# Kernel optimization log

Hardware: AMD Instinct MI355X
Metric: run time of the kernel (lower is better)

## Reference

```python
import jax, jax.numpy as jnp
import numpy as np

N = 50000   # nodes
E = 800000  # random edges (self-loops appended inside reference, as PyG GATConv does)
H = 4       # attention heads
LEAKY_SLOPE = 0.2
BN_EPS = 1e-5


def setup_inputs() -> dict:
    key = jax.random.key(0)
    ks = jax.random.split(key, 24)
    inp = {
        "x": jax.random.normal(ks[0], (N, 128), jnp.float32),
        "edge_index": jax.random.randint(ks[1], (2, E), 0, N, dtype=jnp.int64),
    }
    # layer dims: (in, out_per_head); concat -> out width = H*out
    dims = [(128, 64), (256, 64), (256, 32)]
    i = 2
    for l, (fin, c) in enumerate(dims, start=1):
        sc = 1.0 / np.sqrt(fin)
        inp[f"W{l}"] = jax.random.normal(ks[i], (fin, H * c), jnp.float32) * sc; i += 1
        inp[f"a_src{l}"] = jax.random.normal(ks[i], (H, c), jnp.float32) * 0.1; i += 1
        inp[f"a_dst{l}"] = jax.random.normal(ks[i], (H, c), jnp.float32) * 0.1; i += 1
        inp[f"b{l}"] = jnp.zeros((H * c,), jnp.float32)
    # batch norm params for the two non-final layers (width = 64*4 = 256)
    for l in (1, 2):
        inp[f"gamma{l}"] = jnp.ones((256,), jnp.float32)
        inp[f"beta{l}"] = jnp.zeros((256,), jnp.float32)
    return inp


def _gat_layer(x, src, dst, W, a_src, a_dst, b, heads):
    n = x.shape[0]
    h = (x @ W).reshape(n, heads, -1)                      # [N,H,C]
    al_s = jnp.sum(h * a_src, axis=-1)                     # [N,H]
    al_d = jnp.sum(h * a_dst, axis=-1)                     # [N,H]
    e = jax.nn.leaky_relu(al_s[src] + al_d[dst], LEAKY_SLOPE)  # [Etot,H]
    # numerically-stable edge softmax over incoming edges per destination
    m = jax.ops.segment_max(e, dst, num_segments=n)
    e = jnp.exp(e - m[dst])
    s = jax.ops.segment_sum(e, dst, num_segments=n)
    alpha = e / (s[dst] + 1e-16)                           # [Etot,H]
    msg = alpha[:, :, None] * h[src]                       # [Etot,H,C]
    out = jax.ops.segment_sum(msg, dst, num_segments=n)    # [N,H,C]
    out = out.reshape(n, -1) + b
    return jax.nn.relu(out)  # GAT_NET applies relu after conv


def _batch_norm(x, gamma, beta):
    mean = jnp.mean(x, axis=0)
    var = jnp.var(x, axis=0)  # biased, matches torch BN training normalization
    return (x - mean) * jax.lax.rsqrt(var + BN_EPS) * gamma + beta


def reference(x, edge_index, W1, a_src1, a_dst1, b1, gamma1, beta1,
              W2, a_src2, a_dst2, b2, gamma2, beta2,
              W3, a_src3, a_dst3, b3):
    n = x.shape[0]
    loop = jnp.arange(n, dtype=edge_index.dtype)
    src = jnp.concatenate([edge_index[0], loop])  # add self-loops (PyG default)
    dst = jnp.concatenate([edge_index[1], loop])

    h = _gat_layer(x, src, dst, W1, a_src1, a_dst1, b1, H)
    # outer F.relu is a no-op after GAT_NET's internal relu, kept implicitly
    h = _batch_norm(h, gamma1, beta1)

    h = _gat_layer(h, src, dst, W2, a_src2, a_dst2, b2, H)
    h = _batch_norm(h, gamma2, beta2)

    return _gat_layer(h, src, dst, W3, a_src3, a_dst3, b3, H)
```

## Files before the change

### kernel.cpp

```cpp
#include <hip/hip_runtime.h>
#include <hip/hip_bf16.h>

constexpr int NN   = 50000;
constexpr int EE   = 800000;
constexpr int ETOT = EE + NN;
constexpr int NP   = 50048;
constexpr int NBLK = (NN + 255) / 256;
constexpr float SLOPE  = 0.2f;
constexpr float EPS_BN = 1e-5f;

typedef __attribute__((ext_vector_type(8))) short bf16x8;
typedef __attribute__((ext_vector_type(4))) float f32x4;

__device__ inline float bf2f(unsigned short u) {
    union { unsigned int i; float f; } c; c.i = ((unsigned int)u) << 16; return c.f;
}

__device__ inline void gload16(const __hip_bfloat16* g, __hip_bfloat16* l) {
    __builtin_amdgcn_global_load_lds(
        (const __attribute__((address_space(1))) unsigned int*)g,
        (__attribute__((address_space(3))) unsigned int*)l, 16, 0, 0);
}


__global__ __launch_bounds__(256) void count_kernel(const int* __restrict__ ei,
                                                    int* __restrict__ cnt) {
    int j = blockIdx.x * 256 + threadIdx.x;
    if (j >= ETOT) return;
    int dst = (j < EE) ? ei[EE + j] : (j - EE);
    atomicAdd(&cnt[dst], 1);
}

__global__ __launch_bounds__(256) void scanA_kernel(const int* __restrict__ cnt,
                                                    int* __restrict__ off,
                                                    int* __restrict__ bsum) {
    int b = blockIdx.x, t = threadIdx.x;
    int i = b * 256 + t;
    int v = (i < NN) ? cnt[i] : 0;
    int lane = t & 63, w = t >> 6;
    int x = v;
    #pragma unroll
    for (int o = 1; o < 64; o <<= 1) { int y = __shfl_up(x, o); if (lane >= o) x += y; }
    __shared__ int ws[4];
    if (lane == 63) ws[w] = x;
    __syncthreads();
    int wo = 0;
    for (int k = 0; k < w; ++k) wo += ws[k];
    int incl = x + wo;
    if (i < NN) off[i] = incl - v;
    if (t == 255) bsum[b] = incl;
}

__global__ __launch_bounds__(256) void scanB_kernel(const int* __restrict__ bsum,
                                                    int* __restrict__ bexc,
                                                    int* __restrict__ off) {
    int t = threadIdx.x;
    int v = (t < NBLK) ? bsum[t] : 0;
    int lane = t & 63, w = t >> 6;
    int x = v;
    #pragma unroll
    for (int o = 1; o < 64; o <<= 1) { int y = __shfl_up(x, o); if (lane >= o) x += y; }
    __shared__ int ws[4];
    if (lane == 63) ws[w] = x;
    __syncthreads();
    int wo = 0;
    for (int k = 0; k < w; ++k) wo += ws[k];
    int incl = x + wo;
    if (t < NBLK) bexc[t] = incl - v;
    if (t == 255) off[NN] = incl;
}

__global__ __launch_bounds__(256) void scanC_kernel(const int* __restrict__ bexc,
                                                    int* __restrict__ off,
                                                    int* __restrict__ cur) {
    int i = blockIdx.x * 256 + threadIdx.x;
    if (i >= NN) return;
    int v = off[i] + bexc[blockIdx.x];
    off[i] = v;
    cur[i] = v;
}

__global__ __launch_bounds__(256) void fill_kernel(const int* __restrict__ ei,
                                                   int* __restrict__ cursor,
                                                   int* __restrict__ ssrc) {
    int j = blockIdx.x * 256 + threadIdx.x;
    if (j >= ETOT) return;
    int src, dst;
    if (j < EE) { src = ei[j]; dst = ei[EE + j]; }
    else        { src = dst = j - EE; }
    int pos = atomicAdd(&cursor[dst], 1);
    ssrc[pos] = src;
}

template <int F, bool BN>
__global__ __launch_bounds__(256) void cast_kernel(const float* __restrict__ X,
                                                   const float* __restrict__ scale,
                                                   const float* __restrict__ shift,
                                                   __hip_bfloat16* __restrict__ Xbf) {
    long idx = (long)blockIdx.x * 256 + threadIdx.x;
    long e0 = idx * 8;
    if (e0 >= (long)NP * F) return;
    int row = (int)(e0 / F);
    int col = (int)(e0 % F);
    __hip_bfloat16 o[8];
    if (row < NN) {
        float4 v0 = *reinterpret_cast<const float4*>(X + (size_t)row * F + col);
        float4 v1 = *reinterpret_cast<const float4*>(X + (size_t)row * F + col + 4);
        if (BN) {
            float4 s0 = *reinterpret_cast<const float4*>(scale + col);
            float4 s1 = *reinterpret_cast<const float4*>(scale + col + 4);
            float4 t0 = *reinterpret_cast<const float4*>(shift + col);
            float4 t1 = *reinterpret_cast<const float4*>(shift + col + 4);
            v0.x = v0.x * s0.x + t0.x; v0.y = v0.y * s0.y + t0.y;
            v0.z = v0.z * s0.z + t0.z; v0.w = v0.w * s0.w + t0.w;
            v1.x = v1.x * s1.x + t1.x; v1.y = v1.y * s1.y + t1.y;
            v1.z = v1.z * s1.z + t1.z; v1.w = v1.w * s1.w + t1.w;
        }
        o[0] = __float2bfloat16(v0.x); o[1] = __float2bfloat16(v0.y);
        o[2] = __float2bfloat16(v0.z); o[3] = __float2bfloat16(v0.w);
        o[4] = __float2bfloat16(v1.x); o[5] = __float2bfloat16(v1.y);
        o[6] = __float2bfloat16(v1.z); o[7] = __float2bfloat16(v1.w);
    } else {
        for (int j = 0; j < 8; ++j) o[j] = __float2bfloat16(0.f);
    }
    *reinterpret_cast<bf16x8*>(Xbf + e0) = *reinterpret_cast<bf16x8*>(o);
}

__global__ __launch_bounds__(256) void castw_all_kernel(const float* __restrict__ W1,
                                                        const float* __restrict__ W2,
                                                        const float* __restrict__ W3,
                                                        __hip_bfloat16* __restrict__ WT1,
                                                        __hip_bfloat16* __restrict__ WT2,
                                                        __hip_bfloat16* __restrict__ WT3) {
    int i = blockIdx.x * 256 + threadIdx.x;
    if (i < 32768) {
        int c = i / 128, k = i % 128;
        WT1[i] = __float2bfloat16(W1[(size_t)k * 256 + c]);
    } else if (i < 98304) {
        int j = i - 32768;
        int c = j / 256, k = j % 256;
        WT2[j] = __float2bfloat16(W2[(size_t)k * 256 + c]);
    } else if (i < 131072) {
        int j = i - 98304;
        int c = j / 256, k = j % 256;
        WT3[j] = __float2bfloat16(W3[(size_t)k * 128 + c]);
    }
}

template <int FIN, int WOUT>
__global__ __launch_bounds__(256) void mgemm_kernel(const __hip_bfloat16* __restrict__ A,
                                                    const __hip_bfloat16* __restrict__ BT,
                                                    __hip_bfloat16* __restrict__ Hbf) {
    __shared__ __hip_bfloat16 As[128 * 32];
    __shared__ __hip_bfloat16 Bs[128 * 32];
    int t = threadIdx.x;
    int lane = t & 63, w = t >> 6;
    int row0 = blockIdx.x * 128;
    int col0 = blockIdx.y * 128;
    int wr = w >> 1, wc = w & 1;

    f32x4 acc[4][4];
    #pragma unroll
    for (int m = 0; m < 4; ++m)
        #pragma unroll
        for (int n = 0; n < 4; ++n) acc[m][n] = (f32x4){0.f, 0.f, 0.f, 0.f};

    int srow = w * 32 + (lane >> 2);
    int sbc  = (lane & 3) * 8;
    const __hip_bfloat16* gA0 = A  + (size_t)(row0 + srow)      * FIN + sbc;
    const __hip_bfloat16* gA1 = A  + (size_t)(row0 + srow + 16) * FIN + sbc;
    const __hip_bfloat16* gB0 = BT + (size_t)(col0 + srow)      * FIN + sbc;
    const __hip_bfloat16* gB1 = BT + (size_t)(col0 + srow + 16) * FIN + sbc;
    __hip_bfloat16* lA0 = As + w * 1024;
    __hip_bfloat16* lA1 = As + w * 1024 + 512;
    __hip_bfloat16* lB0 = Bs + w * 1024;
    __hip_bfloat16* lB1 = Bs + w * 1024 + 512;

    int rA = (wr * 64 + (lane & 15)) * 32 + (lane >> 4) * 8;
    int rB = (wc * 64 + (lane & 15)) * 32 + (lane >> 4) * 8;

    for (int k0 = 0; k0 < FIN; k0 += 32) {
        gload16(gA0 + k0, lA0);
        gload16(gA1 + k0, lA1);
        gload16(gB0 + k0, lB0);
        gload16(gB1 + k0, lB1);
        __syncthreads();
        bf16x8 af[4], bfr[4];
        #pragma unroll
        for (int m = 0; m < 4; ++m) af[m]  = *reinterpret_cast<const bf16x8*>(As + rA + m * 16 * 32);
        #pragma unroll
        for (int n = 0; n < 4; ++n) bfr[n] = *reinterpret_cast<const bf16x8*>(Bs + rB + n * 16 * 32);
        #pragma unroll
        for (int m = 0; m < 4; ++m)
            #pragma unroll
            for (int n = 0; n < 4; ++n)
                acc[m][n] = __builtin_amdgcn_mfma_f32_16x16x32_bf16(af[m], bfr[n], acc[m][n], 0, 0, 0);
        __syncthreads();
    }

    #pragma unroll
    for (int m = 0; m < 4; ++m) {
        #pragma unroll
        for (int n = 0; n < 4; ++n) {
            int r = row0 + wr * 64 + m * 16 + (lane >> 4) * 4;
            int c = col0 + wc * 64 + n * 16 + (lane & 15);
            #pragma unroll
            for (int j = 0; j < 4; ++j)
                Hbf[(size_t)(r + j) * WOUT + c] = __float2bfloat16(acc[m][n][j]);
        }
    }
}

template <int HC>
__global__ __launch_bounds__(256) void alsd_kernel(const __hip_bfloat16* __restrict__ Hm,
                                                   const float* __restrict__ a_src,
                                                   const float* __restrict__ a_dst,
                                                   float* __restrict__ als,
                                                   float* __restrict__ ald) {
    constexpr int VW = HC / 64;
    int wid  = threadIdx.x >> 6;
    int lane = threadIdx.x & 63;
    int node = blockIdx.x * 4 + wid;

    float ssum = 0.f, dsum = 0.f;
    if constexpr (VW == 4) {
        ushort4 h4 = *reinterpret_cast<const ushort4*>(Hm + (size_t)node * HC + lane * 4);
        float4 as = *reinterpret_cast<const float4*>(a_src + lane * 4);
        float4 ad = *reinterpret_cast<const float4*>(a_dst + lane * 4);
        float hx = bf2f(h4.x), hy = bf2f(h4.y), hz = bf2f(h4.z), hw = bf2f(h4.w);
        ssum = hx*as.x + hy*as.y + hz*as.z + hw*as.w;
        dsum = hx*ad.x + hy*ad.y + hz*ad.z + hw*ad.w;
    } else {
        ushort2 h2 = *reinterpret_cast<const ushort2*>(Hm + (size_t)node * HC + lane * 2);
        float2 as = *reinterpret_cast<const float2*>(a_src + lane * 2);
        float2 ad = *reinterpret_cast<const float2*>(a_dst + lane * 2);
        float hx = bf2f(h2.x), hy = bf2f(h2.y);
        ssum = hx*as.x + hy*as.y;
        dsum = hx*ad.x + hy*ad.y;
    }
    #pragma unroll
    for (int o = 1; o < 16; o <<= 1) {
        ssum += __shfl_xor(ssum, o);
        dsum += __shfl_xor(dsum, o);
    }
    if ((lane & 15) == 0) {
        int hd = lane >> 4;
        als[node * 4 + hd] = ssum;
        ald[node * 4 + hd] = dsum;
    }
}

template <int HC>
__global__ __launch_bounds__(256) void attn_kernel(const __hip_bfloat16* __restrict__ Hm,
                                                   const int* __restrict__ off,
                                                   const int* __restrict__ ssrc,
                                                   const float* __restrict__ als,
                                                   const float* __restrict__ ald,
                                                   const float* __restrict__ bias,
                                                   float* __restrict__ Out) {
    constexpr int CPL = HC / 16;
    int wid  = threadIdx.x >> 6;
    int lane = threadIdx.x & 63;
    int d    = blockIdx.x * 4 + wid;
    int g    = lane >> 4;
    int q    = lane & 15;
    int head = q >> 2;

    int e0 = off[d], e1 = off[d + 1];
    float aldh = ald[(size_t)d * 4 + head];

    float acc[CPL];
    #pragma unroll
    for (int c = 0; c < CPL; ++c) acc[c] = 0.f;
    float den = 0.f;

    for (int j = e0 + g; j < e1; j += 4) {
        int src = ssrc[j];
        float e = als[(size_t)src * 4 + head] + aldh;
        e = (e > 0.f) ? e : SLOPE * e;
        float wgt = __expf(e);
        den += wgt;
        const __hip_bfloat16* hp = Hm + (size_t)src * HC + q * CPL;
        if constexpr (CPL == 16) {
            bf16x8 v0 = *reinterpret_cast<const bf16x8*>(hp);
            bf16x8 v1 = *reinterpret_cast<const bf16x8*>(hp + 8);
            #pragma unroll
            for (int c = 0; c < 8; ++c) acc[c]     += wgt * bf2f((unsigned short)v0[c]);
            #pragma unroll
            for (int c = 0; c < 8; ++c) acc[8 + c] += wgt * bf2f((unsigned short)v1[c]);
        } else {
            bf16x8 v0 = *reinterpret_cast<const bf16x8*>(hp);
            #pragma unroll
            for (int c = 0; c < 8; ++c) acc[c] += wgt * bf2f((unsigned short)v0[c]);
        }
    }

    #pragma unroll
    for (int c = 0; c < CPL; ++c) {
        acc[c] += __shfl_xor(acc[c], 16);
        acc[c] += __shfl_xor(acc[c], 32);
    }
    den += __shfl_xor(den, 16);
    den += __shfl_xor(den, 32);
    float inv = 1.f / (den + 1e-16f);

    if (g == 0) {
        #pragma unroll
        for (int c4 = 0; c4 < CPL / 4; ++c4) {
            float4 b4 = *reinterpret_cast<const float4*>(bias + q * CPL + c4 * 4);
            float4 o;
            o.x = fmaxf(acc[c4 * 4 + 0] * inv + b4.x, 0.f);
            o.y = fmaxf(acc[c4 * 4 + 1] * inv + b4.y, 0.f);
            o.z = fmaxf(acc[c4 * 4 + 2] * inv + b4.z, 0.f);
            o.w = fmaxf(acc[c4 * 4 + 3] * inv + b4.w, 0.f);
            *reinterpret_cast<float4*>(Out + (size_t)d * HC + q * CPL + c4 * 4) = o;
        }
    }
}

__global__ __launch_bounds__(256) void bnstats_kernel(const float* __restrict__ X,
                                                      float* __restrict__ sums) {
    int c  = threadIdx.x;
    int r0 = blockIdx.x * 200;
    float s = 0.f, q = 0.f;
    for (int r = r0; r < r0 + 200; ++r) {
        float v = X[(size_t)r * 256 + c];
        s += v; q += v * v;
    }
    atomicAdd(&sums[c], s);
    atomicAdd(&sums[256 + c], q);
}

__global__ __launch_bounds__(256) void bnfinal_kernel(const float* __restrict__ sums,
                                                      const float* __restrict__ gamma,
                                                      const float* __restrict__ beta,
                                                      float* __restrict__ scale,
                                                      float* __restrict__ shift) {
    int c = threadIdx.x;
    float mean = sums[c] / (float)NN;
    float var  = sums[256 + c] / (float)NN - mean * mean;
    float inv  = rsqrtf(var + EPS_BN);
    float sc   = gamma[c] * inv;
    scale[c] = sc;
    shift[c] = beta[c] - mean * sc;
}


extern "C" void kernel_launch(void* const* d_in, const int* in_sizes, int n_in,
                              void* d_out, int out_size, void* d_ws, size_t ws_size,
                              hipStream_t stream) {
    const float* x      = (const float*)d_in[0];
    const int*   ei     = (const int*)d_in[1];
    const float* W1     = (const float*)d_in[2];
    const float* a_s1   = (const float*)d_in[3];
    const float* a_d1   = (const float*)d_in[4];
    const float* b1     = (const float*)d_in[5];
    const float* W2     = (const float*)d_in[6];
    const float* a_s2   = (const float*)d_in[7];
    const float* a_d2   = (const float*)d_in[8];
    const float* b2     = (const float*)d_in[9];
    const float* W3     = (const float*)d_in[10];
    const float* a_s3   = (const float*)d_in[11];
    const float* a_d3   = (const float*)d_in[12];
    const float* b3     = (const float*)d_in[13];
    const float* gamma1 = (const float*)d_in[14];
    const float* beta1  = (const float*)d_in[15];
    const float* gamma2 = (const float*)d_in[16];
    const float* beta2  = (const float*)d_in[17];

    char* ws = (char*)d_ws;
    size_t o = 0;
    auto alloc = [&](size_t bytes) -> void* {
        void* p = ws + o;
        o = (o + bytes + 255) & ~size_t(255);
        return p;
    };
    float*           bufB = (float*)alloc((size_t)NN * 256 * 4);
    __hip_bfloat16*  Xbf  = (__hip_bfloat16*)alloc((size_t)NP * 256 * 2);
    __hip_bfloat16*  Hbf  = (__hip_bfloat16*)alloc((size_t)NP * 256 * 2);
    __hip_bfloat16*  WT1  = (__hip_bfloat16*)alloc((size_t)256 * 128 * 2);
    __hip_bfloat16*  WT2  = (__hip_bfloat16*)alloc((size_t)256 * 256 * 2);
    __hip_bfloat16*  WT3  = (__hip_bfloat16*)alloc((size_t)128 * 256 * 2);
    float* als   = (float*)alloc((size_t)NN * 4 * 4);
    float* ald   = (float*)alloc((size_t)NN * 4 * 4);
    float* sums  = (float*)alloc(512 * 4);
    float* scale = (float*)alloc(256 * 4);
    float* shift = (float*)alloc(256 * 4);
    int*   off   = (int*)alloc((size_t)(NN + 1) * 4);
    int*   cur   = (int*)alloc((size_t)NN * 4);
    int*   cnt   = (int*)alloc((size_t)NN * 4);
    int*   bsum  = (int*)alloc((size_t)NBLK * 4);
    int*   bexc  = (int*)alloc((size_t)NBLK * 4);
    int*   ssrc  = (int*)alloc((size_t)ETOT * 4);
    (void)ws_size; (void)in_sizes; (void)n_in; (void)out_size;

    const int EB = (ETOT + 255) / 256;

    hipMemsetAsync(cnt, 0, (size_t)NN * 4, stream);
    count_kernel<<<EB, 256, 0, stream>>>(ei, cnt);
    scanA_kernel<<<NBLK, 256, 0, stream>>>(cnt, off, bsum);
    scanB_kernel<<<1, 256, 0, stream>>>(bsum, bexc, off);
    scanC_kernel<<<NBLK, 256, 0, stream>>>(bexc, off, cur);
    fill_kernel<<<EB, 256, 0, stream>>>(ei, cur, ssrc);

    castw_all_kernel<<<512, 256, 0, stream>>>(W1, W2, W3, WT1, WT2, WT3);

    cast_kernel<128, false><<<(int)(((long)NP * 128 / 8 + 255) / 256), 256, 0, stream>>>(x, nullptr, nullptr, Xbf);
    mgemm_kernel<128, 256><<<dim3(NP / 128, 2), 256, 0, stream>>>(Xbf, WT1, Hbf);
    alsd_kernel<256><<<NN / 4, 256, 0, stream>>>(Hbf, a_s1, a_d1, als, ald);
    attn_kernel<256><<<NN / 4, 256, 0, stream>>>(Hbf, off, ssrc, als, ald, b1, bufB);

    hipMemsetAsync(sums, 0, 512 * 4, stream);
    bnstats_kernel<<<250, 256, 0, stream>>>(bufB, sums);
    bnfinal_kernel<<<1, 256, 0, stream>>>(sums, gamma1, beta1, scale, shift);

    cast_kernel<256, true><<<(int)(((long)NP * 256 / 8 + 255) / 256), 256, 0, stream>>>(bufB, scale, shift, Xbf);
    mgemm_kernel<256, 256><<<dim3(NP / 128, 2), 256, 0, stream>>>(Xbf, WT2, Hbf);
    alsd_kernel<256><<<NN / 4, 256, 0, stream>>>(Hbf, a_s2, a_d2, als, ald);
    attn_kernel<256><<<NN / 4, 256, 0, stream>>>(Hbf, off, ssrc, als, ald, b2, bufB);

    hipMemsetAsync(sums, 0, 512 * 4, stream);
    bnstats_kernel<<<250, 256, 0, stream>>>(bufB, sums);
    bnfinal_kernel<<<1, 256, 0, stream>>>(sums, gamma2, beta2, scale, shift);

    cast_kernel<256, true><<<(int)(((long)NP * 256 / 8 + 255) / 256), 256, 0, stream>>>(bufB, scale, shift, Xbf);
    mgemm_kernel<256, 128><<<dim3(NP / 128, 1), 256, 0, stream>>>(Xbf, WT3, Hbf);
    alsd_kernel<128><<<NN / 4, 256, 0, stream>>>(Hbf, a_s3, a_d3, als, ald);
    attn_kernel<128><<<NN / 4, 256, 0, stream>>>(Hbf, off, ssrc, als, ald, b3, (float*)d_out);
}
```

Before: 413.6 us.

## Fold batch-norm into next-layer weights and emit bf16 attention outputs

Batch-norm scale and shift are folded into the next layer's weight matrix and a per-column bias added in the GEMM epilogue. This removes the separate normalize-and-cast passes over the activation buffer. The intermediate attention outputs are now written directly as bf16, halving their write traffic, and bnstats reads bf16. The attention edge loop is also unrolled by two with independent accumulators to expose more memory-level parallelism. Risks: BN statistics are computed from bf16-rounded values, and the folded weights are rounded to bf16 after scaling.

```diff
diff --git a/kernel.cpp b/kernel.cpp
--- a/kernel.cpp
+++ b/kernel.cpp
@@ -92,30 +92,15 @@
     ssrc[pos] = src;
 }
 
-template <int F, bool BN>
-__global__ __launch_bounds__(256) void cast_kernel(const float* __restrict__ X,
-                                                   const float* __restrict__ scale,
-                                                   const float* __restrict__ shift,
-                                                   __hip_bfloat16* __restrict__ Xbf) {
-    long idx = (long)blockIdx.x * 256 + threadIdx.x;
-    long e0 = idx * 8;
-    if (e0 >= (long)NP * F) return;
-    int row = (int)(e0 / F);
-    int col = (int)(e0 % F);
+__global__ __launch_bounds__(256) void castx_kernel(const float* __restrict__ X,
+                                                    __hip_bfloat16* __restrict__ Xbf) {
+    long e0 = ((long)blockIdx.x * 256 + threadIdx.x) * 8;
+    if (e0 >= (long)NP * 128) return;
+    int row = (int)(e0 / 128);
     __hip_bfloat16 o[8];
     if (row < NN) {
-        float4 v0 = *reinterpret_cast<const float4*>(X + (size_t)row * F + col);
-        float4 v1 = *reinterpret_cast<const float4*>(X + (size_t)row * F + col + 4);
-        if (BN) {
-            float4 s0 = *reinterpret_cast<const float4*>(scale + col);
-            float4 s1 = *reinterpret_cast<const float4*>(scale + col + 4);
-            float4 t0 = *reinterpret_cast<const float4*>(shift + col);
-            float4 t1 = *reinterpret_cast<const float4*>(shift + col + 4);
-            v0.x = v0.x * s0.x + t0.x; v0.y = v0.y * s0.y + t0.y;
-            v0.z = v0.z * s0.z + t0.z; v0.w = v0.w * s0.w + t0.w;
-            v1.x = v1.x * s1.x + t1.x; v1.y = v1.y * s1.y + t1.y;
-            v1.z = v1.z * s1.z + t1.z; v1.w = v1.w * s1.w + t1.w;
-        }
+        float4 v0 = *reinterpret_cast<const float4*>(X + e0);
+        float4 v1 = *reinterpret_cast<const float4*>(X + e0 + 4);
         o[0] = __float2bfloat16(v0.x); o[1] = __float2bfloat16(v0.y);
         o[2] = __float2bfloat16(v0.z); o[3] = __float2bfloat16(v0.w);
         o[4] = __float2bfloat16(v1.x); o[5] = __float2bfloat16(v1.y);
@@ -126,30 +111,41 @@
     *reinterpret_cast<bf16x8*>(Xbf + e0) = *reinterpret_cast<bf16x8*>(o);
 }
 
-__global__ __launch_bounds__(256) void castw_all_kernel(const float* __restrict__ W1,
-                                                        const float* __restrict__ W2,
-                                                        const float* __restrict__ W3,
-                                                        __hip_bfloat16* __restrict__ WT1,
-                                                        __hip_bfloat16* __restrict__ WT2,
-                                                        __hip_bfloat16* __restrict__ WT3) {
+__global__ __launch_bounds__(256) void castw1_kernel(const float* __restrict__ W,
+                                                     __hip_bfloat16* __restrict__ WT) {
     int i = blockIdx.x * 256 + threadIdx.x;
-    if (i < 32768) {
-        int c = i / 128, k = i % 128;
-        WT1[i] = __float2bfloat16(W1[(size_t)k * 256 + c]);
-    } else if (i < 98304) {
-        int j = i - 32768;
-        int c = j / 256, k = j % 256;
-        WT2[j] = __float2bfloat16(W2[(size_t)k * 256 + c]);
-    } else if (i < 131072) {
-        int j = i - 98304;
-        int c = j / 256, k = j % 256;
-        WT3[j] = __float2bfloat16(W3[(size_t)k * 128 + c]);
-    }
+    if (i >= 32768) return;
+    int c = i / 128, k = i % 128;
+    WT[i] = __float2bfloat16(W[(size_t)k * 256 + c]);
 }
 
 template <int FIN, int WOUT>
+__global__ __launch_bounds__(FIN) void foldw_kernel(const float* __restrict__ W,
+                                                    const float* __restrict__ scale,
+                                                    const float* __restrict__ shift,
+                                                    __hip_bfloat16* __restrict__ WTp,
+                                                    float* __restrict__ bb) {
+    int c = blockIdx.x, k = threadIdx.x;
+    float w = W[(size_t)k * WOUT + c];
+    WTp[(size_t)c * FIN + k] = __float2bfloat16(scale[k] * w);
+    float p = shift[k] * w;
+    #pragma unroll
+    for (int o = 1; o < 64; o <<= 1) p += __shfl_xor(p, o);
+    __shared__ float ps[FIN / 64];
+    if ((k & 63) == 0) ps[k >> 6] = p;
+    __syncthreads();
+    if (k == 0) {
+        float s = 0.f;
+        #pragma unroll
+        for (int q = 0; q < FIN / 64; ++q) s += ps[q];
+        bb[c] = s;
+    }
+}
+
+template <int FIN, int WOUT, bool FOLD>
 __global__ __launch_bounds__(256) void mgemm_kernel(const __hip_bfloat16* __restrict__ A,
                                                     const __hip_bfloat16* __restrict__ BT,
+                                                    const float* __restrict__ bb,
                                                     __hip_bfloat16* __restrict__ Hbf) {
     __shared__ __hip_bfloat16 As[128 * 32];
     __shared__ __hip_bfloat16 Bs[128 * 32];
@@ -199,14 +195,15 @@
     }
 
     #pragma unroll
-    for (int m = 0; m < 4; ++m) {
-        #pragma unroll
-        for (int n = 0; n < 4; ++n) {
+    for (int n = 0; n < 4; ++n) {
+        int c = col0 + wc * 64 + n * 16 + (lane & 15);
+        float badd = FOLD ? bb[c] : 0.f;
+        #pragma unroll
+        for (int m = 0; m < 4; ++m) {
             int r = row0 + wr * 64 + m * 16 + (lane >> 4) * 4;
-            int c = col0 + wc * 64 + n * 16 + (lane & 15);
             #pragma unroll
             for (int j = 0; j < 4; ++j)
-                Hbf[(size_t)(r + j) * WOUT + c] = __float2bfloat16(acc[m][n][j]);
+                Hbf[(size_t)(r + j) * WOUT + c] = __float2bfloat16(acc[m][n][j] + badd);
         }
     }
 }
@@ -250,14 +247,14 @@
     }
 }
 
-template <int HC>
+template <int HC, bool OUTBF>
 __global__ __launch_bounds__(256) void attn_kernel(const __hip_bfloat16* __restrict__ Hm,
                                                    const int* __restrict__ off,
                                                    const int* __restrict__ ssrc,
                                                    const float* __restrict__ als,
                                                    const float* __restrict__ ald,
                                                    const float* __restrict__ bias,
-                                                   float* __restrict__ Out) {
+                                                   void* __restrict__ Outv) {
     constexpr int CPL = HC / 16;
     int wid  = threadIdx.x >> 6;
     int lane = threadIdx.x & 63;
@@ -269,31 +266,71 @@
     int e0 = off[d], e1 = off[d + 1];
     float aldh = ald[(size_t)d * 4 + head];
 
+    float acc0[CPL], acc1[CPL];
+    #pragma unroll
+    for (int c = 0; c < CPL; ++c) { acc0[c] = 0.f; acc1[c] = 0.f; }
+    float den0 = 0.f, den1 = 0.f;
+
+    int j = e0 + g;
+    for (; j + 4 < e1; j += 8) {
+        int s0 = ssrc[j];
+        int s1 = ssrc[j + 4];
+        float ea = als[(size_t)s0 * 4 + head] + aldh;
+        ea = (ea > 0.f) ? ea : SLOPE * ea;
+        float eb = als[(size_t)s1 * 4 + head] + aldh;
+        eb = (eb > 0.f) ? eb : SLOPE * eb;
+        float w0 = __expf(ea), w1 = __expf(eb);
+        den0 += w0; den1 += w1;
+        const __hip_bfloat16* hp0 = Hm + (size_t)s0 * HC + q * CPL;
+        const __hip_bfloat16* hp1 = Hm + (size_t)s1 * HC + q * CPL;
+        if constexpr (CPL == 16) {
+            bf16x8 a0 = *reinterpret_cast<const bf16x8*>(hp0);
+            bf16x8 a1 = *reinterpret_cast<const bf16x8*>(hp0 + 8);
+            bf16x8 b0 = *reinterpret_cast<const bf16x8*>(hp1);
+            bf16x8 b1 = *reinterpret_cast<const bf16x8*>(hp1 + 8);
+            #pragma unroll
+            for (int c = 0; c < 8; ++c) {
+                acc0[c]     += w0 * bf2f((unsigned short)a0[c]);
+                acc0[8 + c] += w0 * bf2f((unsigned short)a1[c]);
+                acc1[c]     += w1 * bf2f((unsigned short)b0[c]);
+                acc1[8 + c] += w1 * bf2f((unsigned short)b1[c]);
+            }
+        } else {
+            bf16x8 a0 = *reinterpret_cast<const bf16x8*>(hp0);
+            bf16x8 b0 = *reinterpret_cast<const bf16x8*>(hp1);
+            #pragma unroll
+            for (int c = 0; c < 8; ++c) {
+                acc0[c] += w0 * bf2f((unsigned short)a0[c]);
+                acc1[c] += w1 * bf2f((unsigned short)b0[c]);
+            }
+        }
+    }
+    if (j < e1) {
+        int s0 = ssrc[j];
+        float ea = als[(size_t)s0 * 4 + head] + aldh;
+        ea = (ea > 0.f) ? ea : SLOPE * ea;
+        float w0 = __expf(ea);
+        den0 += w0;
+        const __hip_bfloat16* hp0 = Hm + (size_t)s0 * HC + q * CPL;
+        if constexpr (CPL == 16) {
+            bf16x8 a0 = *reinterpret_cast<const bf16x8*>(hp0);
+            bf16x8 a1 = *reinterpret_cast<const bf16x8*>(hp0 + 8);
+            #pragma unroll
+            for (int c = 0; c < 8; ++c) {
+                acc0[c]     += w0 * bf2f((unsigned short)a0[c]);
+                acc0[8 + c] += w0 * bf2f((unsigned short)a1[c]);
+            }
+        } else {
+            bf16x8 a0 = *reinterpret_cast<const bf16x8*>(hp0);
+            #pragma unroll
+            for (int c = 0; c < 8; ++c) acc0[c] += w0 * bf2f((unsigned short)a0[c]);
+        }
+    }
+
+    float den = den0 + den1;
     float acc[CPL];
     #pragma unroll
-    for (int c = 0; c < CPL; ++c) acc[c] = 0.f;
-    float den = 0.f;
-
-    for (int j = e0 + g; j < e1; j += 4) {
-        int src = ssrc[j];
-        float e = als[(size_t)src * 4 + head] + aldh;
-        e = (e > 0.f) ? e : SLOPE * e;
-        float wgt = __expf(e);
-        den += wgt;
-        const __hip_bfloat16* hp = Hm + (size_t)src * HC + q * CPL;
-        if constexpr (CPL == 16) {
-            bf16x8 v0 = *reinterpret_cast<const bf16x8*>(hp);
-            bf16x8 v1 = *reinterpret_cast<const bf16x8*>(hp + 8);
-            #pragma unroll
-            for (int c = 0; c < 8; ++c) acc[c]     += wgt * bf2f((unsigned short)v0[c]);
-            #pragma unroll
-            for (int c = 0; c < 8; ++c) acc[8 + c] += wgt * bf2f((unsigned short)v1[c]);
-        } else {
-            bf16x8 v0 = *reinterpret_cast<const bf16x8*>(hp);
-            #pragma unroll
-            for (int c = 0; c < 8; ++c) acc[c] += wgt * bf2f((unsigned short)v0[c]);
-        }
-    }
+    for (int c = 0; c < CPL; ++c) acc[c] = acc0[c] + acc1[c];
 
     #pragma unroll
     for (int c = 0; c < CPL; ++c) {
@@ -305,26 +342,40 @@
     float inv = 1.f / (den + 1e-16f);
 
     if (g == 0) {
+        float o[CPL];
         #pragma unroll
         for (int c4 = 0; c4 < CPL / 4; ++c4) {
             float4 b4 = *reinterpret_cast<const float4*>(bias + q * CPL + c4 * 4);
-            float4 o;
-            o.x = fmaxf(acc[c4 * 4 + 0] * inv + b4.x, 0.f);
-            o.y = fmaxf(acc[c4 * 4 + 1] * inv + b4.y, 0.f);
-            o.z = fmaxf(acc[c4 * 4 + 2] * inv + b4.z, 0.f);
-            o.w = fmaxf(acc[c4 * 4 + 3] * inv + b4.w, 0.f);
-            *reinterpret_cast<float4*>(Out + (size_t)d * HC + q * CPL + c4 * 4) = o;
+            o[c4 * 4 + 0] = fmaxf(acc[c4 * 4 + 0] * inv + b4.x, 0.f);
+            o[c4 * 4 + 1] = fmaxf(acc[c4 * 4 + 1] * inv + b4.y, 0.f);
+            o[c4 * 4 + 2] = fmaxf(acc[c4 * 4 + 2] * inv + b4.z, 0.f);
+            o[c4 * 4 + 3] = fmaxf(acc[c4 * 4 + 3] * inv + b4.w, 0.f);
         }
-    }
-}
-
-__global__ __launch_bounds__(256) void bnstats_kernel(const float* __restrict__ X,
+        if constexpr (OUTBF) {
+            __hip_bfloat16 ob[CPL];
+            #pragma unroll
+            for (int c = 0; c < CPL; ++c) ob[c] = __float2bfloat16(o[c]);
+            __hip_bfloat16* op = (__hip_bfloat16*)Outv + (size_t)d * HC + q * CPL;
+            #pragma unroll
+            for (int c8 = 0; c8 < CPL / 8; ++c8)
+                *reinterpret_cast<bf16x8*>(op + c8 * 8) = *reinterpret_cast<bf16x8*>(ob + c8 * 8);
+        } else {
+            float* op = (float*)Outv + (size_t)d * HC + q * CPL;
+            #pragma unroll
+            for (int c4 = 0; c4 < CPL / 4; ++c4)
+                *reinterpret_cast<float4*>(op + c4 * 4) =
+                    make_float4(o[c4*4+0], o[c4*4+1], o[c4*4+2], o[c4*4+3]);
+        }
+    }
+}
+
+__global__ __launch_bounds__(256) void bnstats_kernel(const __hip_bfloat16* __restrict__ X,
                                                       float* __restrict__ sums) {
     int c  = threadIdx.x;
     int r0 = blockIdx.x * 200;
     float s = 0.f, q = 0.f;
     for (int r = r0; r < r0 + 200; ++r) {
-        float v = X[(size_t)r * 256 + c];
+        float v = bf2f(*(const unsigned short*)(X + (size_t)r * 256 + c));
         s += v; q += v * v;
     }
     atomicAdd(&sums[c], s);
@@ -375,12 +426,14 @@
         o = (o + bytes + 255) & ~size_t(255);
         return p;
     };
-    float*           bufB = (float*)alloc((size_t)NN * 256 * 4);
-    __hip_bfloat16*  Xbf  = (__hip_bfloat16*)alloc((size_t)NP * 256 * 2);
+    __hip_bfloat16*  Abf  = (__hip_bfloat16*)alloc((size_t)NP * 256 * 2);
     __hip_bfloat16*  Hbf  = (__hip_bfloat16*)alloc((size_t)NP * 256 * 2);
+    __hip_bfloat16*  Xbf  = (__hip_bfloat16*)alloc((size_t)NP * 128 * 2);
     __hip_bfloat16*  WT1  = (__hip_bfloat16*)alloc((size_t)256 * 128 * 2);
     __hip_bfloat16*  WT2  = (__hip_bfloat16*)alloc((size_t)256 * 256 * 2);
     __hip_bfloat16*  WT3  = (__hip_bfloat16*)alloc((size_t)128 * 256 * 2);
+    float* bb2   = (float*)alloc(256 * 4);
+    float* bb3   = (float*)alloc(128 * 4);
     float* als   = (float*)alloc((size_t)NN * 4 * 4);
     float* ald   = (float*)alloc((size_t)NN * 4 * 4);
     float* sums  = (float*)alloc(512 * 4);
@@ -403,28 +456,27 @@
     scanC_kernel<<<NBLK, 256, 0, stream>>>(bexc, off, cur);
     fill_kernel<<<EB, 256, 0, stream>>>(ei, cur, ssrc);
 
-    castw_all_kernel<<<512, 256, 0, stream>>>(W1, W2, W3, WT1, WT2, WT3);
-
-    cast_kernel<128, false><<<(int)(((long)NP * 128 / 8 + 255) / 256), 256, 0, stream>>>(x, nullptr, nullptr, Xbf);
-    mgemm_kernel<128, 256><<<dim3(NP / 128, 2), 256, 0, stream>>>(Xbf, WT1, Hbf);
+    castw1_kernel<<<128, 256, 0, stream>>>(W1, WT1);
+    castx_kernel<<<(int)(((long)NP * 128 / 8 + 255) / 256), 256, 0, stream>>>(x, Xbf);
+    mgemm_kernel<128, 256, false><<<dim3(NP / 128, 2), 256, 0, stream>>>(Xbf, WT1, nullptr, Hbf);
     alsd_kernel<256><<<NN / 4, 256, 0, stream>>>(Hbf, a_s1, a_d1, als, ald);
-    attn_kernel<256><<<NN / 4, 256, 0, stream>>>(Hbf, off, ssrc, als, ald, b1, bufB);
+    attn_kernel<256, true><<<NN / 4, 256, 0, stream>>>(Hbf, off, ssrc, als, ald, b1, Abf);
 
     hipMemsetAsync(sums, 0, 512 * 4, stream);
-    bnstats_kernel<<<250, 256, 0, stream>>>(bufB, sums);
+    bnstats_kernel<<<250, 256, 0, stream>>>(Abf, sums);
     bnfinal_kernel<<<1, 256, 0, stream>>>(sums, gamma1, beta1, scale, shift);
-
-    cast_kernel<256, true><<<(int)(((long)NP * 256 / 8 + 255) / 256), 256, 0, stream>>>(bufB, scale, shift, Xbf);
-    mgemm_kernel<256, 256><<<dim3(NP / 128, 2), 256, 0, stream>>>(Xbf, WT2, Hbf);
+    foldw_kernel<256, 256><<<256, 256, 0, stream>>>(W2, scale, shift, WT2, bb2);
+
+    mgemm_kernel<256, 256, true><<<dim3(NP / 128, 2), 256, 0, stream>>>(Abf, WT2, bb2, Hbf);
     alsd_kernel<256><<<NN / 4, 256, 0, stream>>>(Hbf, a_s2, a_d2, als, ald);
-    attn_kernel<256><<<NN / 4, 256, 0, stream>>>(Hbf, off, ssrc, als, ald, b2, bufB);
+    attn_kernel<256, true><<<NN / 4, 256, 0, stream>>>(Hbf, off, ssrc, als, ald, b2, Abf);
 
     hipMemsetAsync(sums, 0, 512 * 4, stream);
-    bnstats_kernel<<<250, 256, 0, stream>>>(bufB, sums);
+    bnstats_kernel<<<250, 256, 0, stream>>>(Abf, sums);
     bnfinal_kernel<<<1, 256, 0, stream>>>(sums, gamma2, beta2, scale, shift);
-
-    cast_kernel<256, true><<<(int)(((long)NP * 256 / 8 + 255) / 256), 256, 0, stream>>>(bufB, scale, shift, Xbf);
-    mgemm_kernel<256, 128><<<dim3(NP / 128, 1), 256, 0, stream>>>(Xbf, WT3, Hbf);
+    foldw_kernel<256, 128><<<128, 256, 0, stream>>>(W3, scale, shift, WT3, bb3);
+
+    mgemm_kernel<256, 128, true><<<dim3(NP / 128, 1), 256, 0, stream>>>(Abf, WT3, bb3, Hbf);
     alsd_kernel<128><<<NN / 4, 256, 0, stream>>>(Hbf, a_s3, a_d3, als, ald);
-    attn_kernel<128><<<NN / 4, 256, 0, stream>>>(Hbf, off, ssrc, als, ald, b3, (float*)d_out);
-}
+    attn_kernel<128, false><<<NN / 4, 256, 0, stream>>>(Hbf, off, ssrc, als, ald, b3, d_out);
+}
```

Result: faster. 402.5 us (-2.7%).
